# Kernel optimization log

Hardware: AMD Instinct MI355X
Metric: run time of the kernel (lower is better)

The kernel has to match this reference:

```python
import jax, jax.numpy as jnp
import numpy as np
from jax import lax

INPUT, HIDDEN, LAYERS, ACTIONS = 512, 128, 2, 10
B, T = 512, 256


def _lstm_layer(x_seq, Wih, Whh, bih, bhh):
    """x_seq: [B,T,D] -> (outputs [B,T,H], h_T [B,H], c_T [B,H]). PyTorch gate order i,f,g,o."""
    Bsz = x_seq.shape[0]
    H = Whh.shape[1]
    # Precompute input projection for all timesteps (one big GEMM).
    x_proj = jnp.einsum('btd,gd->btg', x_seq, Wih) + bih + bhh  # [B,T,4H]

    def step(carry, xt):
        h, c = carry
        gates = xt + h @ Whh.T  # [B,4H]
        i, f, g, o = jnp.split(gates, 4, axis=-1)
        c = jax.nn.sigmoid(f) * c + jax.nn.sigmoid(i) * jnp.tanh(g)
        h = jax.nn.sigmoid(o) * jnp.tanh(c)
        return (h, c), h

    init = (jnp.zeros((Bsz, H), x_seq.dtype), jnp.zeros((Bsz, H), x_seq.dtype))
    (hT, cT), hs = lax.scan(step, init, jnp.swapaxes(x_proj, 0, 1))  # hs: [T,B,H]
    return jnp.swapaxes(hs, 0, 1), hT, cT


def setup_inputs() -> dict:
    key = jax.random.key(0)
    ks = jax.random.split(key, 16)
    s_in = 1.0 / np.sqrt(HIDDEN)

    def u(k, shape):
        return jax.random.uniform(k, shape, jnp.float32, -s_in, s_in)

    return {
        'x': jax.random.normal(ks[0], (B, T, INPUT), jnp.float32),
        'Wih0': u(ks[1], (4 * HIDDEN, INPUT)),
        'Whh0': u(ks[2], (4 * HIDDEN, HIDDEN)),
        'bih0': u(ks[3], (4 * HIDDEN,)),
        'bhh0': u(ks[4], (4 * HIDDEN,)),
        'Wih1': u(ks[5], (4 * HIDDEN, HIDDEN)),
        'Whh1': u(ks[6], (4 * HIDDEN, HIDDEN)),
        'bih1': u(ks[7], (4 * HIDDEN,)),
        'bhh1': u(ks[8], (4 * HIDDEN,)),
        'fc1_w': u(ks[9], (HIDDEN // 2, HIDDEN)),
        'fc1_b': u(ks[10], (HIDDEN // 2,)),
        'fc2_w': u(ks[11], (ACTIONS, HIDDEN // 2)),
        'fc2_b': u(ks[12], (ACTIONS,)),
    }


def reference(x, Wih0, Whh0, bih0, bhh0, Wih1, Whh1, bih1, bhh1, fc1_w, fc1_b, fc2_w, fc2_b):
    # Layer 0 (input 512 -> hidden 128); dropout is inference-off (identity).
    h0_seq, h0, c0 = _lstm_layer(x, Wih0, Whh0, bih0, bhh0)
    # Layer 1 (hidden 128 -> hidden 128)
    h1_seq, h1, c1 = _lstm_layer(h0_seq, Wih1, Whh1, bih1, bhh1)
    last = h1_seq[:, -1, :]  # [B,H]
    hid = jax.nn.relu(last @ fc1_w.T + fc1_b)
    logits = hid @ fc2_w.T + fc2_b
    probs = jax.nn.softmax(logits, axis=-1)
    h_n = jnp.stack([h0, h1], axis=0)  # [num_layers,B,H]
    c_n = jnp.stack([c0, c1], axis=0)
    return probs, h_n, c_n
```

## Files before the change

### kernel.cpp

```cpp
#include <hip/hip_runtime.h>
#include <hip/hip_bf16.h>


#define BATCH 512
#define SEQT  256
#define INPUTD 512
#define HID   128
#define GATES 512
#define RB    4
#define SUBS  16
#define NCH   (SEQT / SUBS)

typedef __bf16 bf16_t;
typedef bf16_t bf16x4 __attribute__((ext_vector_type(4)));
typedef bf16_t bf16x8 __attribute__((ext_vector_type(8)));
typedef float  f32x4  __attribute__((ext_vector_type(4)));

__device__ __forceinline__ float sigm(float x) {
    return __builtin_amdgcn_rcpf(1.f + __expf(-x));
}
__device__ __forceinline__ float tanhfast(float x) {
    float xc = fminf(fmaxf(x, -15.f), 15.f);
    float e = __expf(2.f * xc);
    return (e - 1.f) * __builtin_amdgcn_rcpf(e + 1.f);
}

__global__ __launch_bounds__(256) void cvt_weights(
    const float* __restrict__ w0, const float* __restrict__ w1,
    const float* __restrict__ w2, const float* __restrict__ w3,
    bf16_t* __restrict__ o0, bf16_t* __restrict__ o1,
    bf16_t* __restrict__ o2, bf16_t* __restrict__ o3,
    unsigned* __restrict__ flags)
{
    int b = blockIdx.x;
    if (b == 448) {
        uint4 z = make_uint4(0u, 0u, 0u, 0u);
        #pragma unroll
        for (int i = 0; i < 4; ++i)
            ((uint4*)flags)[i * 256 + threadIdx.x] = z;
        return;
    }
    const float* src; bf16_t* dst; long base;
    if (b < 256)      { src = w0; dst = o0; base = (long)b * 256; }
    else if (b < 320) { src = w1; dst = o1; base = (long)(b - 256) * 256; }
    else if (b < 384) { src = w2; dst = o2; base = (long)(b - 320) * 256; }
    else              { src = w3; dst = o3; base = (long)(b - 384) * 256; }
    long i = base + threadIdx.x;
    float4 v = ((const float4*)src)[i];
    bf16x4 r;
    r[0] = (bf16_t)v.x; r[1] = (bf16_t)v.y;
    r[2] = (bf16_t)v.z; r[3] = (bf16_t)v.w;
    ((bf16x4*)dst)[i] = r;
}

__global__ __launch_bounds__(256) void gemm_mfma(
    const float* __restrict__ A, const bf16_t* __restrict__ W,
    const float* __restrict__ b1, const float* __restrict__ b2,
    float* __restrict__ out,
    int K, int tcs, int tcmask, int srcT, int t0)
{
    __shared__ bf16_t As[128 * 32];
    __shared__ bf16_t Bs[128 * 32];
    int tid = threadIdx.x;
    int l = tid & 63;
    int w = tid >> 6;
    int wm = w >> 1, wn = w & 1;
    int bn = blockIdx.x;
    int bm = blockIdx.y;
    int Tc = tcmask + 1;

    long aoff[2], boff[2];
    #pragma unroll
    for (int c = 0; c < 2; ++c) {
        int m = bm * 128 + (tid >> 2) + 64 * c;
        int xr = ((m >> tcs) * srcT) + t0 + (m & tcmask);
        aoff[c] = (long)xr * K + (tid & 3) * 8;
        int n = bn * 128 + (tid >> 2) + 64 * c;
        boff[c] = (long)n * K + (tid & 3) * 8;
    }

    f32x4 acc[4][4];
    #pragma unroll
    for (int i = 0; i < 4; ++i)
        #pragma unroll
        for (int j = 0; j < 4; ++j)
            acc[i][j] = (f32x4){0.f, 0.f, 0.f, 0.f};

    const int rbase = wm * 64 + (l & 15);
    const int cbase = wn * 64 + (l & 15);
    const int kfrag = (l >> 4) * 8;

    for (int kt = 0; kt < K; kt += 32) {
        float4 av[2][2];
        #pragma unroll
        for (int c = 0; c < 2; ++c) {
            av[c][0] = *(const float4*)(A + aoff[c] + kt);
            av[c][1] = *(const float4*)(A + aoff[c] + kt + 4);
        }
        __builtin_amdgcn_global_load_lds(
            (const __attribute__((address_space(1))) void*)(W + boff[0] + kt),
            (__attribute__((address_space(3))) void*)(Bs + tid * 8), 16, 0, 0);
        __builtin_amdgcn_global_load_lds(
            (const __attribute__((address_space(1))) void*)(W + boff[1] + kt),
            (__attribute__((address_space(3))) void*)(Bs + 2048 + tid * 8), 16, 0, 0);
        #pragma unroll
        for (int c = 0; c < 2; ++c) {
            bf16x8 ab;
            ab[0] = (bf16_t)av[c][0].x; ab[1] = (bf16_t)av[c][0].y;
            ab[2] = (bf16_t)av[c][0].z; ab[3] = (bf16_t)av[c][0].w;
            ab[4] = (bf16_t)av[c][1].x; ab[5] = (bf16_t)av[c][1].y;
            ab[6] = (bf16_t)av[c][1].z; ab[7] = (bf16_t)av[c][1].w;
            *(bf16x8*)(As + c * 2048 + tid * 8) = ab;
        }
        __syncthreads();

        bf16x8 af[4], bfr[4];
        #pragma unroll
        for (int i = 0; i < 4; ++i)
            af[i] = *(const bf16x8*)(As + (rbase + i * 16) * 32 + kfrag);
        #pragma unroll
        for (int j = 0; j < 4; ++j)
            bfr[j] = *(const bf16x8*)(Bs + (cbase + j * 16) * 32 + kfrag);

        #pragma unroll
        for (int i = 0; i < 4; ++i)
            #pragma unroll
            for (int j = 0; j < 4; ++j)
                acc[i][j] = __builtin_amdgcn_mfma_f32_16x16x32_bf16(
                    af[i], bfr[j], acc[i][j], 0, 0, 0);
        __syncthreads();
    }

    #pragma unroll
    for (int i = 0; i < 4; ++i) {
        int m0 = bm * 128 + wm * 64 + i * 16 + (l >> 4) * 4;
        #pragma unroll
        for (int j = 0; j < 4; ++j) {
            int n = bn * 128 + wn * 64 + j * 16 + (l & 15);
            float bb = b1[n] + b2[n];
            int hid = n & 127;
            #pragma unroll
            for (int r = 0; r < 4; ++r) {
                int m = m0 + r;
                int b = m >> tcs;
                int t = m & tcmask;
                int br = b >> 2, brow = b & 3;
                out[(((long)br * Tc + t) * 4 + bn) * 512 + brow * 128 + hid] =
                    acc[i][j][r] + bb;
            }
        }
    }
}

#define BARRIER_()                                                             \
    do {                                                                       \
        asm volatile("s_waitcnt lgkmcnt(0)" ::: "memory");                     \
        __builtin_amdgcn_s_barrier();                                          \
        __builtin_amdgcn_sched_barrier(0);                                     \
    } while (0)

#define REC0_STEP(X, t)                                                        \
    {                                                                          \
        bf16x8 a[4];                                                           \
        _Pragma("unroll")                                                      \
        for (int ks = 0; ks < 4; ++ks) {                                       \
            int ba = (col * 256 + ks * 64 + lgroup * 16) ^ ((col & 7) << 4);   \
            a[ks] = *(const bf16x8*)((const char*)h_lds + ba);                 \
        }                                                                      \
        f32x4 acc[4];                                                          \
        _Pragma("unroll")                                                      \
        for (int g = 0; g < 4; ++g) acc[g] = (f32x4){0.f, 0.f, 0.f, 0.f};      \
        _Pragma("unroll")                                                      \
        for (int ks = 0; ks < 4; ++ks)                                         \
            _Pragma("unroll")                                                  \
            for (int g = 0; g < 4; ++g)                                        \
                acc[g] = __builtin_amdgcn_mfma_f32_16x16x32_bf16(              \
                    a[ks], __builtin_bit_cast(bf16x8, wreg[g][ks]), acc[g],    \
                    0, 0, 0);                                                  \
        if (lgroup == 0) {                                                     \
            _Pragma("unroll")                                                  \
            for (int r = 0; r < 4; ++r) {                                      \
                f32x4 v;                                                       \
                v[0] = acc[0][r]; v[1] = acc[1][r];                            \
                v[2] = acc[2][r]; v[3] = acc[3][r];                            \
                *(f32x4*)((char*)g_lds + r * 2048 + coff * 16) = v;            \
            }                                                                  \
        }                                                                      \
        BARRIER_();                                                            \
        {                                                                      \
            f32x4 gv = *(const f32x4*)((const char*)g_lds + tid * 16);         \
            float zi = gv[0] + X.x, zf = gv[1] + X.y;                          \
            float zg = gv[2] + X.z, zo = gv[3] + X.w;                          \
            c = sigm(zf) * c + sigm(zi) * tanhfast(zg);                        \
            h = sigm(zo) * tanhfast(c);                                        \
            *(bf16_t*)((char*)h_lds + hba) = (bf16_t)h;                        \
            h0qp[(long)(t) * 512] = (bf16_t)h;                                 \
        }                                                                      \
        if ((t) + 2 < Tc) {                                                    \
            long o = (long)((t) + 2) * 2048;                                   \
            X.x = xpt[o];        X.y = xpt[o + 512];                           \
            X.z = xpt[o + 1024]; X.w = xpt[o + 1536];                          \
        }                                                                      \
        if (((t) & (SUBS - 1)) == SUBS - 1)                                    \
            asm volatile("s_waitcnt vmcnt(0)" ::: "memory");                   \
        BARRIER_();                                                            \
        if ((((t) & (SUBS - 1)) == SUBS - 1) && tid == 0) {                    \
            __threadfence();                                                   \
            __hip_atomic_store(flagp + ((t) >> 4), 1u, __ATOMIC_RELEASE,       \
                               __HIP_MEMORY_SCOPE_AGENT);                      \
        }                                                                      \
    }

__global__ __launch_bounds__(512, 2) void lstm_dual(
    const float* __restrict__ xp4,
    const bf16_t* __restrict__ Wh0,
    const bf16_t* __restrict__ Wi1,
    const bf16_t* __restrict__ Wh1,
    const float* __restrict__ bih1, const float* __restrict__ bhh1,
    bf16_t* __restrict__ h0q,
    unsigned* __restrict__ flags,
    float* __restrict__ h0st, float* __restrict__ c0st,
    float* __restrict__ h1st, float* __restrict__ c1st,
    int Tc, int first, int subbase)
{
    __shared__ __align__(16) char pool[36 * 1024];
    int tid = threadIdx.x;
    int l = tid & 63;
    int wv = tid >> 6;
    int pair = blockIdx.x & 127;
    int r0 = pair * RB;
    int col = l & 15;
    int lgroup = l >> 4;
    int kreg = lgroup * 8;
    int erow = tid >> 7, ehid = tid & 127;
    const int hba = (erow * 256 + ehid * 2) ^ ((erow & 7) << 4);
    unsigned* flagp = flags + pair * NCH + subbase;

    if (blockIdx.x < 128) {
        bf16_t* h_lds = (bf16_t*)pool;
        float*  g_lds = (float*)(pool + 4096);
        int coff = wv * 16 + col;

        f32x4 wreg[4][4];
        #pragma unroll
        for (int g = 0; g < 4; ++g)
            #pragma unroll
            for (int ks = 0; ks < 4; ++ks)
                wreg[g][ks] = *(const f32x4*)(Wh0 + (long)(g * 128 + coff) * HID
                                              + ks * 32 + kreg);
        #pragma unroll
        for (int g = 0; g < 4; ++g)
            #pragma unroll
            for (int ks = 0; ks < 4; ++ks)
                asm volatile("" : "+a"(wreg[g][ks]));

        float c = first ? 0.f : c0st[(r0 + erow) * HID + ehid];
        float h = first ? 0.f : h0st[(r0 + erow) * HID + ehid];

        ((float2*)h_lds)[tid & 255] = make_float2(0.f, 0.f);
        __syncthreads();
        *(bf16_t*)((char*)h_lds + hba) = (bf16_t)h;
        __syncthreads();

        const float* xpt = xp4 + (long)pair * Tc * 2048 + tid;
        bf16_t* h0qp = h0q + (long)pair * Tc * 512 + (hba >> 1);
        float4 xA, xB;
        xA.x = xpt[0];    xA.y = xpt[512];
        xA.z = xpt[1024]; xA.w = xpt[1536];
        if (Tc > 1) {
            xB.x = xpt[2048];        xB.y = xpt[2048 + 512];
            xB.z = xpt[2048 + 1024]; xB.w = xpt[2048 + 1536];
        } else {
            xB = make_float4(0.f, 0.f, 0.f, 0.f);
        }

        for (int tt = 0; tt < Tc; tt += 2) {
            REC0_STEP(xA, tt)
            REC0_STEP(xB, tt + 1)
        }

        h0st[(r0 + erow) * HID + ehid] = h;
        c0st[(r0 + erow) * HID + ehid] = c;
    } else {
        bf16_t* h0stg = (bf16_t*)pool;
        bf16_t* h1_lds = (bf16_t*)(pool + 16384);
        float*  g1a = (float*)(pool + 20480);
        float*  g1b = (float*)(pool + 28672);
        int isWi = wv < 4;
        int w4 = wv & 3;
        int coff1 = w4 * 32;

        const bf16_t* Wsrc = isWi ? Wi1 : Wh1;
        f32x4 wreg[2][4][4];
        #pragma unroll
        for (int c2 = 0; c2 < 2; ++c2)
            #pragma unroll
            for (int g = 0; g < 4; ++g)
                #pragma unroll
                for (int ks = 0; ks < 4; ++ks)
                    wreg[c2][g][ks] = *(const f32x4*)(
                        Wsrc + (long)(g * 128 + coff1 + c2 * 16 + col) * HID
                        + ks * 32 + kreg);
        #pragma unroll
        for (int c2 = 0; c2 < 2; ++c2)
            #pragma unroll
            for (int g = 0; g < 4; ++g)
                #pragma unroll
                for (int ks = 0; ks < 4; ++ks)
                    asm volatile("" : "+a"(wreg[c2][g][ks]));

        float4 bias1;
        bias1.x = bih1[ehid]       + bhh1[ehid];
        bias1.y = bih1[128 + ehid] + bhh1[128 + ehid];
        bias1.z = bih1[256 + ehid] + bhh1[256 + ehid];
        bias1.w = bih1[384 + ehid] + bhh1[384 + ehid];

        float c1 = first ? 0.f : c1st[(r0 + erow) * HID + ehid];
        float h1 = first ? 0.f : h1st[(r0 + erow) * HID + ehid];

        #pragma unroll
        for (int i = 0; i < 5; ++i)
            ((float2*)pool)[i * 512 + tid] = make_float2(0.f, 0.f);
        __syncthreads();
        *(bf16_t*)((char*)h1_lds + hba) = (bf16_t)h1;
        __syncthreads();

        if (wv == 0) {
            while (__hip_atomic_load(flagp, __ATOMIC_ACQUIRE,
                                     __HIP_MEMORY_SCOPE_AGENT) == 0u)
                __builtin_amdgcn_s_sleep(2);
            __builtin_amdgcn_global_load_lds(
                (const __attribute__((address_space(1))) void*)(
                    h0q + (long)pair * Tc * 512 + l * 8),
                (__attribute__((address_space(3))) void*)h0stg, 16, 0, 0);
            if (Tc > 1)
                __builtin_amdgcn_global_load_lds(
                    (const __attribute__((address_space(1))) void*)(
                        h0q + ((long)pair * Tc + 1) * 512 + l * 8),
                    (__attribute__((address_space(3))) void*)(h0stg + 2048),
                    16, 0, 0);
            asm volatile("s_waitcnt vmcnt(0)" ::: "memory");
        }
        __syncthreads();

        for (int t = 0; t < Tc; ++t) {
            if (t + 2 < Tc && wv == (t & 3)) {
                if (((t + 2) & (SUBS - 1)) == 0) {
                    unsigned* fp = flagp + ((t + 2) >> 4);
                    while (__hip_atomic_load(fp, __ATOMIC_ACQUIRE,
                                             __HIP_MEMORY_SCOPE_AGENT) == 0u)
                        __builtin_amdgcn_s_sleep(2);
                }
                __builtin_amdgcn_global_load_lds(
                    (const __attribute__((address_space(1))) void*)(
                        h0q + ((long)pair * Tc + t + 2) * 512 + l * 8),
                    (__attribute__((address_space(3))) void*)(
                        h0stg + ((t + 2) & 3) * 2048), 16, 0, 0);
            }

            const char* asrc = isWi
                ? (const char*)(h0stg + (t & 3) * 2048)
                : (const char*)h1_lds;
            bf16x8 a[4];
            #pragma unroll
            for (int ks = 0; ks < 4; ++ks) {
                int ba = (col * 256 + ks * 64 + lgroup * 16) ^ ((col & 7) << 4);
                a[ks] = *(const bf16x8*)(asrc + ba);
            }
            float* gdst = isWi ? g1a : g1b;
            #pragma unroll
            for (int c2 = 0; c2 < 2; ++c2) {
                f32x4 acc[4];
                #pragma unroll
                for (int g = 0; g < 4; ++g) acc[g] = (f32x4){0.f, 0.f, 0.f, 0.f};
                #pragma unroll
                for (int ks = 0; ks < 4; ++ks)
                    #pragma unroll
                    for (int g = 0; g < 4; ++g)
                        acc[g] = __builtin_amdgcn_mfma_f32_16x16x32_bf16(
                            a[ks], __builtin_bit_cast(bf16x8, wreg[c2][g][ks]),
                            acc[g], 0, 0, 0);
                if (lgroup == 0) {
                    #pragma unroll
                    for (int r = 0; r < 4; ++r) {
                        f32x4 v;
                        v[0] = acc[0][r]; v[1] = acc[1][r];
                        v[2] = acc[2][r]; v[3] = acc[3][r];
                        *(f32x4*)((char*)gdst + r * 2048 +
                                  (coff1 + c2 * 16 + col) * 16) = v;
                    }
                }
            }
            BARRIER_();

            {
                f32x4 gva = *(const f32x4*)((const char*)g1a + tid * 16);
                f32x4 gvb = *(const f32x4*)((const char*)g1b + tid * 16);
                float zi = gva[0] + gvb[0] + bias1.x;
                float zf = gva[1] + gvb[1] + bias1.y;
                float zg = gva[2] + gvb[2] + bias1.z;
                float zo = gva[3] + gvb[3] + bias1.w;
                c1 = sigm(zf) * c1 + sigm(zi) * tanhfast(zg);
                h1 = sigm(zo) * tanhfast(c1);
                *(bf16_t*)((char*)h1_lds + hba) = (bf16_t)h1;
            }
            if (t + 1 < Tc && wv == ((t + 3) & 3))
                asm volatile("s_waitcnt vmcnt(0)" ::: "memory");
            BARRIER_();
        }

        h1st[(r0 + erow) * HID + ehid] = h1;
        c1st[(r0 + erow) * HID + ehid] = c1;
    }
}

__global__ __launch_bounds__(128) void fc_head(
    const float* __restrict__ h0st, const float* __restrict__ c0st,
    const float* __restrict__ h1st, const float* __restrict__ c1st,
    const float* __restrict__ fc1w, const float* __restrict__ fc1b,
    const float* __restrict__ fc2w, const float* __restrict__ fc2b,
    float* __restrict__ out)
{
    __shared__ float h1_s[HID];
    __shared__ float hid_s[64];
    __shared__ float log_s[10];
    int t = threadIdx.x;
    int b = blockIdx.x;

    h1_s[t] = h1st[b * HID + t];
    __syncthreads();

    if (t < 64) {
        float a = fc1b[t];
        const float* wrow = fc1w + t * HID;
        #pragma unroll 4
        for (int k = 0; k < HID; ++k) a = fmaf(wrow[k], h1_s[k], a);
        hid_s[t] = fmaxf(a, 0.f);
    }
    __syncthreads();

    if (t < 10) {
        float a = fc2b[t];
        const float* wrow = fc2w + t * 64;
        #pragma unroll 4
        for (int k = 0; k < 64; ++k) a = fmaf(wrow[k], hid_s[k], a);
        log_s[t] = a;
    }
    __syncthreads();

    if (t == 0) {
        float m = log_s[0];
        #pragma unroll
        for (int j = 1; j < 10; ++j) m = fmaxf(m, log_s[j]);
        float e[10];
        float s = 0.f;
        #pragma unroll
        for (int j = 0; j < 10; ++j) { e[j] = __expf(log_s[j] - m); s += e[j]; }
        float inv = __builtin_amdgcn_rcpf(s);
        #pragma unroll
        for (int j = 0; j < 10; ++j) out[b * 10 + j] = e[j] * inv;
    }

    float* hn = out + BATCH * 10;
    float* cn = hn + 2 * BATCH * HID;
    hn[b * HID + t] = h0st[b * HID + t];
    hn[BATCH * HID + b * HID + t] = h1_s[t];
    cn[b * HID + t] = c0st[b * HID + t];
    cn[BATCH * HID + b * HID + t] = c1st[b * HID + t];
}

extern "C" void kernel_launch(void* const* d_in, const int* in_sizes, int n_in,
                              void* d_out, int out_size, void* d_ws, size_t ws_size,
                              hipStream_t stream) {
    const float* x    = (const float*)d_in[0];
    const float* Wih0 = (const float*)d_in[1];
    const float* Whh0 = (const float*)d_in[2];
    const float* bih0 = (const float*)d_in[3];
    const float* bhh0 = (const float*)d_in[4];
    const float* Wih1 = (const float*)d_in[5];
    const float* Whh1 = (const float*)d_in[6];
    const float* bih1 = (const float*)d_in[7];
    const float* bhh1 = (const float*)d_in[8];
    const float* fc1w = (const float*)d_in[9];
    const float* fc1b = (const float*)d_in[10];
    const float* fc2w = (const float*)d_in[11];
    const float* fc2b = (const float*)d_in[12];
    float* out = (float*)d_out;

    int Tc = SEQT;
    while (Tc > SUBS) {
        size_t need = (size_t)BATCH * Tc * GATES * 4
                    + ((size_t)GATES * INPUTD + 3 * (size_t)GATES * HID) * 2
                    + (size_t)128 * Tc * 512 * 2
                    + 4 * (size_t)BATCH * HID * 4
                    + 128 * NCH * 4 + 512;
        if (need <= ws_size) break;
        Tc >>= 1;
    }
    int tcs = __builtin_ctz((unsigned)Tc);

    float*    xp   = (float*)d_ws;
    bf16_t*   wb0  = (bf16_t*)(xp + (size_t)BATCH * Tc * GATES);
    bf16_t*   wb1  = wb0 + (size_t)GATES * INPUTD;
    bf16_t*   wh0b = wb1 + (size_t)GATES * HID;
    bf16_t*   wh1b = wh0b + (size_t)GATES * HID;
    bf16_t*   h0q  = wh1b + (size_t)GATES * HID;
    float*    h0st = (float*)(h0q + (size_t)128 * Tc * 512);
    float*    c0st = h0st + (size_t)BATCH * HID;
    float*    h1st = c0st + (size_t)BATCH * HID;
    float*    c1st = h1st + (size_t)BATCH * HID;
    unsigned* flags = (unsigned*)(c1st + (size_t)BATCH * HID);

    cvt_weights<<<449, 256, 0, stream>>>(Wih0, Wih1, Whh0, Whh1,
                                         wb0, wb1, wh0b, wh1b, flags);

    int nchunk = SEQT / Tc;
    dim3 gemm_grid(GATES / 128, (BATCH * Tc) / 128);

    for (int ci = 0; ci < nchunk; ++ci) {
        gemm_mfma<<<gemm_grid, 256, 0, stream>>>(
            x, wb0, bih0, bhh0, xp, INPUTD, tcs, Tc - 1, SEQT, ci * Tc);
        lstm_dual<<<256, 512, 0, stream>>>(
            xp, wh0b, wb1, wh1b, bih1, bhh1, h0q, flags,
            h0st, c0st, h1st, c1st, Tc, ci == 0, ci * (Tc / SUBS));
    }

    fc_head<<<BATCH, 128, 0, stream>>>(
        h0st, c0st, h1st, c1st, fc1w, fc1b, fc2w, fc2b, out);
}
```

Baseline: 575.8 us.

## Apply LSTM gates in MFMA lanes and double-buffer h to drop a barrier

```diff
diff --git a/kernel.cpp b/kernel.cpp
--- a/kernel.cpp
+++ b/kernel.cpp
@@ -159,13 +159,15 @@
         __builtin_amdgcn_sched_barrier(0);                                     \
     } while (0)
 
-#define REC0_STEP(X, t)                                                        \
+#define REC0_STEP(XN, t)                                                       \
     {                                                                          \
+        const char* rb = (const char*)h_lds + ((t) & 1) * 4096;                \
+        char* wb2 = (char*)h_lds + ((((t) & 1)) ^ 1) * 4096;                   \
         bf16x8 a[4];                                                           \
         _Pragma("unroll")                                                      \
         for (int ks = 0; ks < 4; ++ks) {                                       \
             int ba = (col * 256 + ks * 64 + lgroup * 16) ^ ((col & 7) << 4);   \
-            a[ks] = *(const bf16x8*)((const char*)h_lds + ba);                 \
+            a[ks] = *(const bf16x8*)(rb + ba);                                 \
         }                                                                      \
         f32x4 acc[4];                                                          \
         _Pragma("unroll")                                                      \
@@ -178,28 +180,27 @@
                     a[ks], __builtin_bit_cast(bf16x8, wreg[g][ks]), acc[g],    \
                     0, 0, 0);                                                  \
         if (lgroup == 0) {                                                     \
+            bf16_t* h0qt = h0qbase + (long)(t) * 512;                          \
             _Pragma("unroll")                                                  \
             for (int r = 0; r < 4; ++r) {                                      \
-                f32x4 v;                                                       \
-                v[0] = acc[0][r]; v[1] = acc[1][r];                            \
-                v[2] = acc[2][r]; v[3] = acc[3][r];                            \
-                *(f32x4*)((char*)g_lds + r * 2048 + coff * 16) = v;            \
+                float zi = acc[0][r] + XN[r];                                  \
+                float zf = acc[1][r] + XN[4 + r];                              \
+                float zg = acc[2][r] + XN[8 + r];                              \
+                float zo = acc[3][r] + XN[12 + r];                             \
+                c_[r] = sigm(zf) * c_[r] + sigm(zi) * tanhfast(zg);            \
+                hv_[r] = sigm(zo) * tanhfast(c_[r]);                           \
+                int ba2 = (r * 256 + coff * 2) ^ (r << 4);                     \
+                *(bf16_t*)(wb2 + ba2) = (bf16_t)hv_[r];                        \
+                h0qt[ba2 >> 1] = (bf16_t)hv_[r];                               \
             }                                                                  \
-        }                                                                      \
-        BARRIER_();                                                            \
-        {                                                                      \
-            f32x4 gv = *(const f32x4*)((const char*)g_lds + tid * 16);         \
-            float zi = gv[0] + X.x, zf = gv[1] + X.y;                          \
-            float zg = gv[2] + X.z, zo = gv[3] + X.w;                          \
-            c = sigm(zf) * c + sigm(zi) * tanhfast(zg);                        \
-            h = sigm(zo) * tanhfast(c);                                        \
-            *(bf16_t*)((char*)h_lds + hba) = (bf16_t)h;                        \
-            h0qp[(long)(t) * 512] = (bf16_t)h;                                 \
-        }                                                                      \
-        if ((t) + 2 < Tc) {                                                    \
-            long o = (long)((t) + 2) * 2048;                                   \
-            X.x = xpt[o];        X.y = xpt[o + 512];                           \
-            X.z = xpt[o + 1024]; X.w = xpt[o + 1536];                          \
+            if ((t) + 2 < Tc) {                                                \
+                const float* xs = xpt + (long)((t) + 2) * 2048;                \
+                _Pragma("unroll")                                              \
+                for (int g = 0; g < 4; ++g)                                    \
+                    _Pragma("unroll")                                          \
+                    for (int r = 0; r < 4; ++r)                                \
+                        XN[g * 4 + r] = xs[g * 512 + r * 128 + coff];          \
+            }                                                                  \
         }                                                                      \
         if (((t) & (SUBS - 1)) == SUBS - 1)                                    \
             asm volatile("s_waitcnt vmcnt(0)" ::: "memory");                   \
@@ -223,7 +224,7 @@
     float* __restrict__ h1st, float* __restrict__ c1st,
     int Tc, int first, int subbase)
 {
-    __shared__ __align__(16) char pool[36 * 1024];
+    __shared__ __align__(16) char pool[24 * 1024];
     int tid = threadIdx.x;
     int l = tid & 63;
     int wv = tid >> 6;
@@ -232,14 +233,11 @@
     int col = l & 15;
     int lgroup = l >> 4;
     int kreg = lgroup * 8;
-    int erow = tid >> 7, ehid = tid & 127;
-    const int hba = (erow * 256 + ehid * 2) ^ ((erow & 7) << 4);
+    int coff = wv * 16 + col;
     unsigned* flagp = flags + pair * NCH + subbase;
 
     if (blockIdx.x < 128) {
         bf16_t* h_lds = (bf16_t*)pool;
-        float*  g_lds = (float*)(pool + 4096);
-        int coff = wv * 16 + col;
 
         f32x4 wreg[4][4];
         #pragma unroll
@@ -254,75 +252,94 @@
             for (int ks = 0; ks < 4; ++ks)
                 asm volatile("" : "+a"(wreg[g][ks]));
 
-        float c = first ? 0.f : c0st[(r0 + erow) * HID + ehid];
-        float h = first ? 0.f : h0st[(r0 + erow) * HID + ehid];
-
-        ((float2*)h_lds)[tid & 255] = make_float2(0.f, 0.f);
-        __syncthreads();
-        *(bf16_t*)((char*)h_lds + hba) = (bf16_t)h;
-        __syncthreads();
-
-        const float* xpt = xp4 + (long)pair * Tc * 2048 + tid;
-        bf16_t* h0qp = h0q + (long)pair * Tc * 512 + (hba >> 1);
-        float4 xA, xB;
-        xA.x = xpt[0];    xA.y = xpt[512];
-        xA.z = xpt[1024]; xA.w = xpt[1536];
-        if (Tc > 1) {
-            xB.x = xpt[2048];        xB.y = xpt[2048 + 512];
-            xB.z = xpt[2048 + 1024]; xB.w = xpt[2048 + 1536];
-        } else {
-            xB = make_float4(0.f, 0.f, 0.f, 0.f);
+        ((f32x4*)pool)[tid] = (f32x4){0.f, 0.f, 0.f, 0.f};
+        __syncthreads();
+
+        float c_[4] = {0.f, 0.f, 0.f, 0.f};
+        float hv_[4] = {0.f, 0.f, 0.f, 0.f};
+        if (lgroup == 0) {
+            #pragma unroll
+            for (int r = 0; r < 4; ++r) {
+                if (!first) {
+                    hv_[r] = h0st[(r0 + r) * HID + coff];
+                    c_[r]  = c0st[(r0 + r) * HID + coff];
+                }
+                int ba2 = (r * 256 + coff * 2) ^ (r << 4);
+                *(bf16_t*)((char*)h_lds + ba2) = (bf16_t)hv_[r];
+            }
+        }
+        __syncthreads();
+
+        const float* xpt = xp4 + (long)pair * Tc * 2048;
+        bf16_t* h0qbase = h0q + (long)pair * Tc * 512;
+        float XA[16], XB[16];
+        if (lgroup == 0) {
+            #pragma unroll
+            for (int g = 0; g < 4; ++g)
+                #pragma unroll
+                for (int r = 0; r < 4; ++r) {
+                    XA[g * 4 + r] = xpt[g * 512 + r * 128 + coff];
+                    XB[g * 4 + r] = (Tc > 1)
+                        ? xpt[2048 + g * 512 + r * 128 + coff] : 0.f;
+                }
         }
 
         for (int tt = 0; tt < Tc; tt += 2) {
-            REC0_STEP(xA, tt)
-            REC0_STEP(xB, tt + 1)
-        }
-
-        h0st[(r0 + erow) * HID + ehid] = h;
-        c0st[(r0 + erow) * HID + ehid] = c;
+            REC0_STEP(XA, tt)
+            REC0_STEP(XB, tt + 1)
+        }
+
+        if (lgroup == 0) {
+            #pragma unroll
+            for (int r = 0; r < 4; ++r) {
+                h0st[(r0 + r) * HID + coff] = hv_[r];
+                c0st[(r0 + r) * HID + coff] = c_[r];
+            }
+        }
     } else {
         bf16_t* h0stg = (bf16_t*)pool;
         bf16_t* h1_lds = (bf16_t*)(pool + 16384);
-        float*  g1a = (float*)(pool + 20480);
-        float*  g1b = (float*)(pool + 28672);
-        int isWi = wv < 4;
-        int w4 = wv & 3;
-        int coff1 = w4 * 32;
-
-        const bf16_t* Wsrc = isWi ? Wi1 : Wh1;
-        f32x4 wreg[2][4][4];
-        #pragma unroll
-        for (int c2 = 0; c2 < 2; ++c2)
-            #pragma unroll
-            for (int g = 0; g < 4; ++g)
-                #pragma unroll
-                for (int ks = 0; ks < 4; ++ks)
-                    wreg[c2][g][ks] = *(const f32x4*)(
-                        Wsrc + (long)(g * 128 + coff1 + c2 * 16 + col) * HID
-                        + ks * 32 + kreg);
-        #pragma unroll
-        for (int c2 = 0; c2 < 2; ++c2)
-            #pragma unroll
-            for (int g = 0; g < 4; ++g)
-                #pragma unroll
-                for (int ks = 0; ks < 4; ++ks)
-                    asm volatile("" : "+a"(wreg[c2][g][ks]));
-
-        float4 bias1;
-        bias1.x = bih1[ehid]       + bhh1[ehid];
-        bias1.y = bih1[128 + ehid] + bhh1[128 + ehid];
-        bias1.z = bih1[256 + ehid] + bhh1[256 + ehid];
-        bias1.w = bih1[384 + ehid] + bhh1[384 + ehid];
-
-        float c1 = first ? 0.f : c1st[(r0 + erow) * HID + ehid];
-        float h1 = first ? 0.f : h1st[(r0 + erow) * HID + ehid];
-
-        #pragma unroll
-        for (int i = 0; i < 5; ++i)
-            ((float2*)pool)[i * 512 + tid] = make_float2(0.f, 0.f);
-        __syncthreads();
-        *(bf16_t*)((char*)h1_lds + hba) = (bf16_t)h1;
+
+        f32x4 wI[4][4], wH[4][4];
+        #pragma unroll
+        for (int g = 0; g < 4; ++g)
+            #pragma unroll
+            for (int ks = 0; ks < 4; ++ks) {
+                long o = (long)(g * 128 + coff) * HID + ks * 32 + kreg;
+                wI[g][ks] = *(const f32x4*)(Wi1 + o);
+                wH[g][ks] = *(const f32x4*)(Wh1 + o);
+            }
+        #pragma unroll
+        for (int g = 0; g < 4; ++g)
+            #pragma unroll
+            for (int ks = 0; ks < 4; ++ks) {
+                asm volatile("" : "+a"(wI[g][ks]));
+                asm volatile("" : "+a"(wH[g][ks]));
+            }
+
+        float bias_[4];
+        #pragma unroll
+        for (int g = 0; g < 4; ++g)
+            bias_[g] = bih1[g * 128 + coff] + bhh1[g * 128 + coff];
+
+        #pragma unroll
+        for (int i = 0; i < 3; ++i)
+            ((f32x4*)pool)[i * 512 + tid] = (f32x4){0.f, 0.f, 0.f, 0.f};
+        __syncthreads();
+
+        float c_[4] = {0.f, 0.f, 0.f, 0.f};
+        float hv_[4] = {0.f, 0.f, 0.f, 0.f};
+        if (lgroup == 0) {
+            #pragma unroll
+            for (int r = 0; r < 4; ++r) {
+                if (!first) {
+                    hv_[r] = h1st[(r0 + r) * HID + coff];
+                    c_[r]  = c1st[(r0 + r) * HID + coff];
+                }
+                int ba2 = (r * 256 + coff * 2) ^ (r << 4);
+                *(bf16_t*)((char*)h1_lds + ba2) = (bf16_t)hv_[r];
+            }
+        }
         __syncthreads();
 
         if (wv == 0) {
@@ -358,59 +375,60 @@
                         h0stg + ((t + 2) & 3) * 2048), 16, 0, 0);
             }
 
-            const char* asrc = isWi
-                ? (const char*)(h0stg + (t & 3) * 2048)
-                : (const char*)h1_lds;
-            bf16x8 a[4];
+            const char* sb = (const char*)h0stg + (t & 3) * 4096;
+            const char* rb = (const char*)h1_lds + (t & 1) * 4096;
+            char* wb2 = (char*)h1_lds + ((t & 1) ^ 1) * 4096;
+
+            bf16x8 a0[4], a1[4];
             #pragma unroll
             for (int ks = 0; ks < 4; ++ks) {
                 int ba = (col * 256 + ks * 64 + lgroup * 16) ^ ((col & 7) << 4);
-                a[ks] = *(const bf16x8*)(asrc + ba);
-            }
-            float* gdst = isWi ? g1a : g1b;
-            #pragma unroll
-            for (int c2 = 0; c2 < 2; ++c2) {
-                f32x4 acc[4];
+                a0[ks] = *(const bf16x8*)(sb + ba);
+                a1[ks] = *(const bf16x8*)(rb + ba);
+            }
+            f32x4 acc[4];
+            #pragma unroll
+            for (int g = 0; g < 4; ++g) acc[g] = (f32x4){0.f, 0.f, 0.f, 0.f};
+            #pragma unroll
+            for (int ks = 0; ks < 4; ++ks)
                 #pragma unroll
-                for (int g = 0; g < 4; ++g) acc[g] = (f32x4){0.f, 0.f, 0.f, 0.f};
+                for (int g = 0; g < 4; ++g)
+                    acc[g] = __builtin_amdgcn_mfma_f32_16x16x32_bf16(
+                        a0[ks], __builtin_bit_cast(bf16x8, wI[g][ks]), acc[g],
+                        0, 0, 0);
+            #pragma unroll
+            for (int ks = 0; ks < 4; ++ks)
                 #pragma unroll
-                for (int ks = 0; ks < 4; ++ks)
-                    #pragma unroll
-                    for (int g = 0; g < 4; ++g)
-                        acc[g] = __builtin_amdgcn_mfma_f32_16x16x32_bf16(
-                            a[ks], __builtin_bit_cast(bf16x8, wreg[c2][g][ks]),
-                            acc[g], 0, 0, 0);
-                if (lgroup == 0) {
-                    #pragma unroll
-                    for (int r = 0; r < 4; ++r) {
-                        f32x4 v;
-                        v[0] = acc[0][r]; v[1] = acc[1][r];
-                        v[2] = acc[2][r]; v[3] = acc[3][r];
-                        *(f32x4*)((char*)gdst + r * 2048 +
-                                  (coff1 + c2 * 16 + col) * 16) = v;
-                    }
+                for (int g = 0; g < 4; ++g)
+                    acc[g] = __builtin_amdgcn_mfma_f32_16x16x32_bf16(
+                        a1[ks], __builtin_bit_cast(bf16x8, wH[g][ks]), acc[g],
+                        0, 0, 0);
+
+            if (lgroup == 0) {
+                #pragma unroll
+                for (int r = 0; r < 4; ++r) {
+                    float zi = acc[0][r] + bias_[0];
+                    float zf = acc[1][r] + bias_[1];
+                    float zg = acc[2][r] + bias_[2];
+                    float zo = acc[3][r] + bias_[3];
+                    c_[r] = sigm(zf) * c_[r] + sigm(zi) * tanhfast(zg);
+                    hv_[r] = sigm(zo) * tanhfast(c_[r]);
+                    int ba2 = (r * 256 + coff * 2) ^ (r << 4);
+                    *(bf16_t*)(wb2 + ba2) = (bf16_t)hv_[r];
                 }
-            }
-            BARRIER_();
-
-            {
-                f32x4 gva = *(const f32x4*)((const char*)g1a + tid * 16);
-                f32x4 gvb = *(const f32x4*)((const char*)g1b + tid * 16);
-                float zi = gva[0] + gvb[0] + bias1.x;
-                float zf = gva[1] + gvb[1] + bias1.y;
-                float zg = gva[2] + gvb[2] + bias1.z;
-                float zo = gva[3] + gvb[3] + bias1.w;
-                c1 = sigm(zf) * c1 + sigm(zi) * tanhfast(zg);
-                h1 = sigm(zo) * tanhfast(c1);
-                *(bf16_t*)((char*)h1_lds + hba) = (bf16_t)h1;
             }
             if (t + 1 < Tc && wv == ((t + 3) & 3))
                 asm volatile("s_waitcnt vmcnt(0)" ::: "memory");
             BARRIER_();
         }
 
-        h1st[(r0 + erow) * HID + ehid] = h1;
-        c1st[(r0 + erow) * HID + ehid] = c1;
+        if (lgroup == 0) {
+            #pragma unroll
+            for (int r = 0; r < 4; ++r) {
+                h1st[(r0 + r) * HID + coff] = hv_[r];
+                c1st[(r0 + r) * HID + coff] = c_[r];
+            }
+        }
     }
 }
 
```

New measurement: 701.6 us. 1.22x slower.
